# Kernel tuning notes

Measured on AMD Instinct MI355X. Metric: run time of the kernel, lower is better.

Reference implementation:

```python
import jax, jax.numpy as jnp
import numpy as np

B, S, D, H = 2, 2048, 2048, 16
HD = D // H  # head_dim = 128


def setup_inputs() -> dict:
    key = jax.random.key(0)
    k1, k2, k3, k4, k5, k6 = jax.random.split(key, 6)
    scale = 1.0 / np.sqrt(D)
    return {
        "hidden_states": jax.random.normal(k1, (B, S, D), dtype=jnp.float32),
        "attention_mask": jnp.ones((B, S), dtype=jnp.int32),
        "wq": jax.random.normal(k2, (D, D), dtype=jnp.float32) * scale,
        "wk": jax.random.normal(k3, (D, D), dtype=jnp.float32) * scale,
        "wv": jax.random.normal(k4, (D, D), dtype=jnp.float32) * scale,
        "wo": jax.random.normal(k5, (D, D), dtype=jnp.float32) * scale,
        "bo": jax.random.normal(k6, (D,), dtype=jnp.float32) * 0.01,
    }


def reference(hidden_states, attention_mask, wq, wk, wv, wo, bo):
    b, s, d = hidden_states.shape
    # QKV projections (no bias), split heads -> [B, S, H, HD]
    q = (hidden_states @ wq).reshape(b, s, H, HD)
    k = (hidden_states @ wk).reshape(b, s, H, HD)
    v = (hidden_states @ wv).reshape(b, s, H, HD)

    # combined causal + padding mask -> [B, 1, S, S]
    causal = jnp.tril(jnp.ones((s, s), dtype=bool))[None, None]
    pad = (attention_mask > 0)[:, None, None, :]  # [B,1,1,S]
    mask = jnp.logical_and(causal, pad)

    big_neg = jnp.finfo(hidden_states.dtype).min
    bias = jnp.where(mask, 0.0, big_neg).astype(hidden_states.dtype)

    # scaled dot-product attention (flax dot_product_attention scales by 1/sqrt(head_dim))
    scores = jnp.einsum("bqhd,bkhd->bhqk", q, k) / jnp.sqrt(jnp.asarray(HD, hidden_states.dtype))
    probs = jax.nn.softmax(scores + bias, axis=-1)
    ctx = jnp.einsum("bhqk,bkhd->bqhd", probs, v).reshape(b, s, d)

    return ctx @ wo + bo
```

## Files before the change

kernel.cpp:

```cpp
#include <hip/hip_runtime.h>
#include <hip/hip_bf16.h>
#include <stdint.h>

#define Bv 2
#define Sv 2048
#define Dv 2048
#define Hv 16
#define HDv 128
#define Mv (Bv*Sv)

typedef __attribute__((ext_vector_type(8))) short short8;
typedef __attribute__((ext_vector_type(4))) short short4v;
typedef __attribute__((ext_vector_type(4))) float f32x4;

__device__ __forceinline__ unsigned short bf16_rne(float f) {
    union { float f; uint32_t u; } c; c.f = f;
    uint32_t u = c.u;
    u += 0x7fffu + ((u >> 16) & 1u);
    return (unsigned short)(u >> 16);
}

__device__ __forceinline__ uint32_t cvt_pk_bf16(float lo, float hi) {
    uint32_t r;
    asm("v_cvt_pk_bf16_f32 %0, %1, %2" : "=v"(r) : "v"(lo), "v"(hi));
    return r;
}

__device__ __forceinline__ void gload16(const void* g, void* l) {
    __builtin_amdgcn_global_load_lds((const __attribute__((address_space(1))) void*)g,
                                     (__attribute__((address_space(3))) void*)l, 16, 0, 0);
}

#define BARRIER() asm volatile("s_barrier" ::: "memory")
#define LGKM0()   do { asm volatile("s_waitcnt lgkmcnt(0)" ::: "memory"); \
                       __builtin_amdgcn_sched_barrier(0); } while (0)

__global__ void cvt_x_kernel(const float* __restrict__ x, unsigned short* __restrict__ xb) {
    int i = (blockIdx.x * 256 + threadIdx.x) * 4;
    float4 v = *(const float4*)(x + i);
    short4v o;
    o[0] = (short)bf16_rne(v.x);
    o[1] = (short)bf16_rne(v.y);
    o[2] = (short)bf16_rne(v.z);
    o[3] = (short)bf16_rne(v.w);
    *(short4v*)(xb + i) = o;
}

__global__ void cvt_wt_kernel(const float* __restrict__ w0, const float* __restrict__ w1,
                              const float* __restrict__ w2, const float* __restrict__ w3,
                              unsigned short* __restrict__ wt) {
    __shared__ unsigned short t[64][65];
    int z = blockIdx.z;
    const float* w = (z == 0) ? w0 : (z == 1) ? w1 : (z == 2) ? w2 : w3;
    unsigned short* o = wt + (size_t)z * Dv * Dv;
    int k0 = blockIdx.x * 64, n0 = blockIdx.y * 64;
    for (int i = threadIdx.x; i < 4096; i += 256) {
        int r = i >> 6, c = i & 63;
        t[r][c] = bf16_rne(w[(size_t)(k0 + r) * Dv + n0 + c]);
    }
    __syncthreads();
    for (int i = threadIdx.x; i < 4096; i += 256) {
        int r = i >> 6, c = i & 63;
        o[(size_t)(n0 + r) * Dv + k0 + c] = t[c][r];
    }
}

__global__ void vt_kernel(const unsigned short* __restrict__ V, unsigned short* __restrict__ VT) {
    __shared__ unsigned short t[64 * 64];
    const int tid = threadIdx.x;
    const int b = blockIdx.z;
    const int s0 = blockIdx.x * 64, c0 = blockIdx.y * 64;
    const unsigned short* Vb = V + (size_t)b * Sv * Dv;
    unsigned short* VTb = VT + (size_t)b * Dv * Sv;
    #pragma unroll
    for (int ii = 0; ii < 2; ++ii) {
        int i = tid + ii * 256;
        int r = i >> 3, ch = i & 7;
        short8 v = *(const short8*)&Vb[(size_t)(s0 + r) * Dv + c0 + ch * 8];
        *(short8*)&t[r * 64 + ((ch ^ (r & 7)) << 3)] = v;
    }
    __syncthreads();
    #pragma unroll
    for (int ii = 0; ii < 2; ++ii) {
        int o = tid + ii * 256;
        int orow = o >> 3, och = o & 7;
        short8 v;
        #pragma unroll
        for (int j = 0; j < 8; ++j) {
            int r = och * 8 + j;
            int c = orow;
            v[j] = (short)t[r * 64 + ((((c >> 3) ^ (r & 7)) << 3) | (c & 7))];
        }
        *(short8*)&VTb[(size_t)(c0 + orow) * Sv + s0 + och * 8] = v;
    }
}

__global__ __launch_bounds__(512, 2) void gemm8ph_kernel(
    const unsigned short* __restrict__ A,
    const unsigned short* __restrict__ WtBase,
    unsigned short* __restrict__ CbBase)
{
    extern __shared__ unsigned short lds[];
    const int tid = threadIdx.x;
    const int wv = tid >> 6, ln = tid & 63;
    const int lr = ln & 15, lg = ln >> 4;
    const int wm = wv >> 2, wn = wv & 3;

    const int bid = blockIdx.x;
    const int xcd = bid & 7, idx = bid >> 3;
    const int n_idx = xcd * 3 + idx / 16;
    const int m_idx = idx % 16;
    const int m0 = m_idx * 256, n0g = n_idx * 256;

    const int lrow = wv * 8 + (ln >> 3);
    const int lcol = ((ln & 7) ^ (ln >> 3)) << 3;
    const unsigned short* Ag = A      + (size_t)(m0  + lrow) * Dv + lcol;
    const unsigned short* Bg = WtBase + (size_t)(n0g + lrow) * Dv + lcol;

    auto SH = [&](int T, int isB, int h) {
        const unsigned short* src = (isB ? Bg : Ag) + (size_t)(h * 128) * Dv + T * 64;
        unsigned short* dst = &lds[(T & 1) * 32768 + isB * 16384 + h * 8192 + wv * 512];
        gload16(src, dst);
        gload16(src + (size_t)64 * Dv, dst + 4096);
    };

    const int axk = lr & 7;
    auto RDA = [&](int buf, int fm, int ks) {
        return *(const short8*)&lds[buf * 32768 + (wm * 128 + fm * 16 + lr) * 64 + (((ks * 4 + lg) ^ axk) << 3)];
    };
    auto RDB = [&](int buf, int fn, int ks) {
        return *(const short8*)&lds[buf * 32768 + 16384 + (wn * 64 + fn * 16 + lr) * 64 + (((ks * 4 + lg) ^ axk) << 3)];
    };

    f32x4 acc[8][4];
    #pragma unroll
    for (int fm = 0; fm < 8; fm++)
        #pragma unroll
        for (int fn = 0; fn < 4; fn++)
            acc[fm][fn] = (f32x4){0.f, 0.f, 0.f, 0.f};

    SH(0, 0, 0); SH(0, 0, 1); SH(0, 1, 0); SH(0, 1, 1);
    SH(1, 1, 0); SH(1, 0, 0);
    asm volatile("s_waitcnt vmcnt(4)" ::: "memory");
    BARRIER();

    short8 af[8], b0[4], b1[4];
    const int NT2 = 16;

    #define MFMA_BLK(FN0, FN1, BARR) do {                                              \
        __builtin_amdgcn_s_setprio(1);                                                 \
        _Pragma("unroll")                                                              \
        for (int fm = 0; fm < 8; fm++) {                                               \
            acc[fm][FN0] = __builtin_amdgcn_mfma_f32_16x16x32_bf16(af[fm], BARR[FN0], acc[fm][FN0], 0, 0, 0); \
            acc[fm][FN1] = __builtin_amdgcn_mfma_f32_16x16x32_bf16(af[fm], BARR[FN1], acc[fm][FN1], 0, 0, 0); \
        }                                                                              \
        __builtin_amdgcn_s_setprio(0);                                                 \
    } while (0)

    for (int i = 0; i < NT2; ++i) {
        const int Tb = 2 * i + 1;
        const bool more = (i + 1 < NT2);

        #pragma unroll
        for (int fm = 0; fm < 8; fm++) af[fm] = RDA(0, fm, 0);
        #pragma unroll
        for (int fn = 0; fn < 4; fn++) b0[fn] = RDB(0, fn, 0);
        SH(Tb, 0, 1);
        BARRIER(); LGKM0();
        MFMA_BLK(0, 1, b0);
        BARRIER();

        #pragma unroll
        for (int fn = 0; fn < 4; fn++) b1[fn] = RDB(0, fn, 1);
        SH(Tb, 1, 1);
        BARRIER(); LGKM0();
        MFMA_BLK(2, 3, b0);
        BARRIER();

        #pragma unroll
        for (int fm = 0; fm < 8; fm++) af[fm] = RDA(0, fm, 1);
        if (more) SH(Tb + 1, 1, 0);
        BARRIER(); LGKM0();
        MFMA_BLK(0, 1, b1);
        BARRIER();

        if (more) SH(Tb + 1, 0, 0);
        BARRIER(); LGKM0();
        MFMA_BLK(2, 3, b1);
        if (more) asm volatile("s_waitcnt vmcnt(4)" ::: "memory");
        else      asm volatile("s_waitcnt vmcnt(0)" ::: "memory");
        BARRIER();

        #pragma unroll
        for (int fm = 0; fm < 8; fm++) af[fm] = RDA(1, fm, 0);
        #pragma unroll
        for (int fn = 0; fn < 4; fn++) b0[fn] = RDB(1, fn, 0);
        if (more) SH(Tb + 1, 0, 1);
        BARRIER(); LGKM0();
        MFMA_BLK(0, 1, b0);
        BARRIER();

        #pragma unroll
        for (int fn = 0; fn < 4; fn++) b1[fn] = RDB(1, fn, 1);
        if (more) SH(Tb + 1, 1, 1);
        BARRIER(); LGKM0();
        MFMA_BLK(2, 3, b0);
        BARRIER();

        #pragma unroll
        for (int fm = 0; fm < 8; fm++) af[fm] = RDA(1, fm, 1);
        if (more) SH(Tb + 2, 1, 0);
        BARRIER(); LGKM0();
        MFMA_BLK(0, 1, b1);
        BARRIER();

        if (more) SH(Tb + 2, 0, 0);
        BARRIER(); LGKM0();
        MFMA_BLK(2, 3, b1);
        if (more) {
            asm volatile("s_waitcnt vmcnt(4)" ::: "memory");
            BARRIER();
        }
    }
    #undef MFMA_BLK

    const int z = n0g >> 11;
    unsigned short* Cz = CbBase + (size_t)z * Mv * Dv;
    const int ncl = (n0g & 2047) + wn * 64;
    #pragma unroll
    for (int fm = 0; fm < 8; fm++)
        #pragma unroll
        for (int fn = 0; fn < 4; fn++) {
            int row = m0 + wm * 128 + fm * 16 + lg * 4;
            int col = ncl + fn * 16 + lr;
            #pragma unroll
            for (int r = 0; r < 4; r++)
                Cz[(size_t)(row + r) * Dv + col] = bf16_rne(acc[fm][fn][r]);
        }
}

__global__ __launch_bounds__(512, 2) void gemm8_kernel(
    const unsigned short* __restrict__ A,
    const unsigned short* __restrict__ WtBase,
    float* __restrict__ Cf,
    const float* __restrict__ bias)
{
    extern __shared__ unsigned short lds[];
    const int tid = threadIdx.x;
    const int wv = tid >> 6, ln = tid & 63;
    const int lr = ln & 15, lg = ln >> 4;
    const int wm = wv >> 2, wn = wv & 3;

    const int bid = blockIdx.x;
    const int xcd = bid & 7, idx = bid >> 3;
    const int n_idx = xcd;
    const int m_idx = idx;
    const int m0 = m_idx * 128;
    const int n0g = n_idx * 256;
    const int NT = Dv / 64;

    const int srow = ln >> 3;
    const int swz = ((ln & 7) ^ srow) << 3;
    const unsigned short* Ab = A      + (size_t)(m0  + wv * 8 + srow) * Dv + swz;
    const unsigned short* Bb = WtBase + (size_t)(n0g + wv * 8 + srow) * Dv + swz;

    auto STAGE_A = [&](int t, int d) {
        const unsigned short* g = Ab + t * 64;
        #pragma unroll
        for (int j = 0; j < 2; ++j)
            gload16(g + (size_t)(j * 64) * Dv, &lds[d * 24576 + (j * 64 + wv * 8) * 64]);
    };
    auto STAGE_B = [&](int t, int d) {
        const unsigned short* g = Bb + t * 64;
        #pragma unroll
        for (int j = 0; j < 4; ++j)
            gload16(g + (size_t)(j * 64) * Dv, &lds[d * 24576 + 8192 + (j * 64 + wv * 8) * 64]);
    };

    const int aro = (wm * 64 + lr) * 64;
    const int bro = (wn * 64 + lr) * 64;
    const int ach0 = ((lg ^ (lr & 7)) << 3);
    const int ach1 = (((4 + lg) ^ (lr & 7)) << 3);

    f32x4 acc[4][4];
    #pragma unroll
    for (int mi = 0; mi < 4; mi++)
        #pragma unroll
        for (int ni = 0; ni < 4; ni++)
            acc[mi][ni] = (f32x4){0.f, 0.f, 0.f, 0.f};

    STAGE_A(0, 0); STAGE_B(0, 0);
    STAGE_A(1, 1); STAGE_B(1, 1);
    asm volatile("s_waitcnt vmcnt(6)" ::: "memory");
    BARRIER();

    for (int t = 0; t < NT; ++t) {
        const int d = t % 3, d2 = (t + 2) % 3;
        const unsigned short* la = &lds[d * 24576];
        const unsigned short* lb = &lds[d * 24576 + 8192];

        short8 af[4][2], bf0[2][2];
        #pragma unroll
        for (int mi = 0; mi < 4; mi++) {
            af[mi][0] = *(const short8*)&la[aro + mi * 1024 + ach0];
            af[mi][1] = *(const short8*)&la[aro + mi * 1024 + ach1];
        }
        #pragma unroll
        for (int ni = 0; ni < 2; ni++) {
            bf0[ni][0] = *(const short8*)&lb[bro + ni * 1024 + ach0];
            bf0[ni][1] = *(const short8*)&lb[bro + ni * 1024 + ach1];
        }
        if (t + 2 < NT) STAGE_A(t + 2, d2);
        BARRIER();
        __builtin_amdgcn_s_setprio(1);
        #pragma unroll
        for (int mi = 0; mi < 4; mi++)
            #pragma unroll
            for (int ni = 0; ni < 2; ni++) {
                acc[mi][ni] = __builtin_amdgcn_mfma_f32_16x16x32_bf16(af[mi][0], bf0[ni][0], acc[mi][ni], 0, 0, 0);
                acc[mi][ni] = __builtin_amdgcn_mfma_f32_16x16x32_bf16(af[mi][1], bf0[ni][1], acc[mi][ni], 0, 0, 0);
            }
        __builtin_amdgcn_s_setprio(0);

        short8 bf1[2][2];
        #pragma unroll
        for (int ni = 0; ni < 2; ni++) {
            bf1[ni][0] = *(const short8*)&lb[bro + (ni + 2) * 1024 + ach0];
            bf1[ni][1] = *(const short8*)&lb[bro + (ni + 2) * 1024 + ach1];
        }
        if (t + 2 < NT) STAGE_B(t + 2, d2);
        asm volatile("s_waitcnt vmcnt(6)" ::: "memory");
        BARRIER();
        __builtin_amdgcn_s_setprio(1);
        #pragma unroll
        for (int mi = 0; mi < 4; mi++)
            #pragma unroll
            for (int ni = 0; ni < 2; ni++) {
                acc[mi][ni + 2] = __builtin_amdgcn_mfma_f32_16x16x32_bf16(af[mi][0], bf1[ni][0], acc[mi][ni + 2], 0, 0, 0);
                acc[mi][ni + 2] = __builtin_amdgcn_mfma_f32_16x16x32_bf16(af[mi][1], bf1[ni][1], acc[mi][ni + 2], 0, 0, 0);
            }
        __builtin_amdgcn_s_setprio(0);
    }

    #pragma unroll
    for (int mi = 0; mi < 4; mi++)
        #pragma unroll
        for (int ni = 0; ni < 4; ni++) {
            int row = m0 + wm * 64 + mi * 16 + lg * 4;
            int col = n0g + wn * 64 + ni * 16 + lr;
            float bv = bias[col];
            #pragma unroll
            for (int r = 0; r < 4; r++)
                Cf[(size_t)(row + r) * Dv + col] = acc[mi][ni][r] + bv;
        }
}

__global__ __launch_bounds__(512) void attn_kernel(
    const unsigned short* __restrict__ Q, const unsigned short* __restrict__ K,
    const unsigned short* __restrict__ VT, const int* __restrict__ pmask,
    unsigned short* __restrict__ CTX)
{
    __shared__ unsigned short lK[2][64 * 128];
    __shared__ unsigned short lVt[2][128 * 64];
    __shared__ int lPmB[2][64];
    __shared__ int lPmOk[2];

    const int tid = threadIdx.x, wv = tid >> 6, ln = tid & 63;
    const int lr = ln & 15, lg = ln >> 4;
    const int L = blockIdx.x;
    const int bh = (L & 7) * 4 + ((L >> 3) & 3);
    const int b = bh >> 4, h = bh & 15;
    const int v = L >> 5;
    const int qidx = (v < 8) ? (15 - v) : (v - 8);
    const int q0 = qidx * 128;
    const int qw0 = q0 + wv * 16;
    const size_t hoff  = (size_t)b * Sv * Dv + (size_t)h * HDv;
    const size_t vtoff = ((size_t)b * Dv + (size_t)h * HDv) * Sv;

    short8 qf[4];
    #pragma unroll
    for (int ds = 0; ds < 4; ds++)
        qf[ds] = *(const short8*)&Q[hoff + (size_t)(qw0 + lr) * Dv + ds * 32 + lg * 8];

    size_t koff[2], voff[2];
    #pragma unroll
    for (int ii = 0; ii < 2; ++ii) {
        int slot = ii * 512 + wv * 64 + ln;
        int krow = slot >> 4, kch = slot & 15;
        koff[ii] = hoff + (size_t)krow * Dv + ((kch ^ (krow & 7)) << 3);
        int vrow = slot >> 3, vch = slot & 7;
        voff[ii] = vtoff + (size_t)vrow * Sv + ((vch ^ (vrow & 7)) << 3);
    }

    auto STAGE = [&](int t, int buf) {
        const size_t kadd = (size_t)(t << 6) * Dv;
        const int vadd = t << 6;
        unsigned short* kb = &lK[buf][0];
        unsigned short* vb = &lVt[buf][0];
        #pragma unroll
        for (int ii = 0; ii < 2; ++ii) {
            gload16(K + koff[ii] + kadd, kb + (ii * 512 + wv * 64) * 8);
            gload16(VT + voff[ii] + vadd, vb + (ii * 512 + wv * 64) * 8);
        }
        if (wv == 0) {
            int pmv = pmask[b * Sv + (t << 6) + ln];
            lPmB[buf][ln] = pmv;
            unsigned long long bal = __ballot(pmv != 0);
            if (ln == 0) lPmOk[buf] = (bal == ~0ull) ? 1 : 0;
        }
    };

    f32x4 acc[8];
    #pragma unroll
    for (int n = 0; n < 8; n++) acc[n] = (f32x4){0.f, 0.f, 0.f, 0.f};
    float mrow = -3.0e38f, lrow = 0.f;
    const float CS = 0.12751744f;
    const int qg = qw0 + lr;
    const int nt = (q0 >> 6) + 2;
    const int srcA = lr + ((lg & 1) << 5);
    const int srcB = srcA + 16;
    const bool hiSel = (lg >= 2);

    auto TILE = [&](int t, int buf, auto CAUSAL_c) {
        constexpr bool CAUSAL = decltype(CAUSAL_c)::value;
        const int kv0 = t << 6;
        const unsigned short* kb = &lK[buf][0];
        const unsigned short* vb = &lVt[buf][0];

        f32x4 st[4];
        #pragma unroll
        for (int t2 = 0; t2 < 4; ++t2) st[t2] = (f32x4){0.f, 0.f, 0.f, 0.f};
        __builtin_amdgcn_s_setprio(1);
        #pragma unroll
        for (int t2 = 0; t2 < 4; ++t2) {
            const int krow = t2 * 16 + lr;
            #pragma unroll
            for (int ds = 0; ds < 4; ++ds) {
                const int ch = ds * 4 + lg;
                short8 kf = *(const short8*)&kb[krow * 128 + ((ch ^ (krow & 7)) << 3)];
                st[t2] = __builtin_amdgcn_mfma_f32_16x16x32_bf16(kf, qf[ds], st[t2], 0, 0, 0);
            }
        }
        __builtin_amdgcn_s_setprio(0);

        float sv[4][4];
        float rmax;
        if constexpr (CAUSAL) {
            const int* pm = &lPmB[buf][0];
            #pragma unroll
            for (int t2 = 0; t2 < 4; ++t2)
                #pragma unroll
                for (int r = 0; r < 4; ++r) {
                    int kvl = t2 * 16 + lg * 4 + r;
                    bool ok = ((kv0 + kvl) <= qg) && (pm[kvl] != 0);
                    sv[t2][r] = ok ? st[t2][r] * CS : -1.0e30f;
                }
            rmax = sv[0][0];
            #pragma unroll
            for (int t2 = 0; t2 < 4; ++t2)
                #pragma unroll
                for (int r = 0; r < 4; ++r) rmax = fmaxf(rmax, sv[t2][r]);
            rmax = fmaxf(rmax, __shfl_xor(rmax, 16, 64));
            rmax = fmaxf(rmax, __shfl_xor(rmax, 32, 64));
        } else {
            rmax = st[0][0];
            #pragma unroll
            for (int t2 = 0; t2 < 4; ++t2)
                #pragma unroll
                for (int r = 0; r < 4; ++r) rmax = fmaxf(rmax, st[t2][r]);
            rmax = fmaxf(rmax, __shfl_xor(rmax, 16, 64));
            rmax = fmaxf(rmax, __shfl_xor(rmax, 32, 64));
            rmax *= CS;
        }

        if (!__all(rmax - mrow <= 8.0f)) {
            float mn = fmaxf(mrow, rmax);
            float alpha = exp2f(mrow - mn);
            mrow = mn;
            lrow *= alpha;
            #pragma unroll
            for (int n = 0; n < 8; n++)
                #pragma unroll
                for (int r = 0; r < 4; r++) acc[n][r] *= alpha;
        }

        float p[4][4]; float psum = 0.f;
        if constexpr (CAUSAL) {
            #pragma unroll
            for (int t2 = 0; t2 < 4; ++t2)
                #pragma unroll
                for (int r = 0; r < 4; ++r) {
                    float e = exp2f(sv[t2][r] - mrow);
                    p[t2][r] = (sv[t2][r] > -5.0e29f) ? e : 0.f;
                    psum += p[t2][r];
                }
        } else {
            if (lPmOk[buf]) {
                #pragma unroll
                for (int t2 = 0; t2 < 4; ++t2)
                    #pragma unroll
                    for (int r = 0; r < 4; ++r) {
                        p[t2][r] = exp2f(fmaf(st[t2][r], CS, -mrow));
                        psum += p[t2][r];
                    }
            } else {
                const int* pm = &lPmB[buf][0];
                #pragma unroll
                for (int t2 = 0; t2 < 4; ++t2)
                    #pragma unroll
                    for (int r = 0; r < 4; ++r) {
                        int kvl = t2 * 16 + lg * 4 + r;
                        float e = exp2f(fmaf(st[t2][r], CS, -mrow));
                        p[t2][r] = (pm[kvl] != 0) ? e : 0.f;
                        psum += p[t2][r];
                    }
            }
        }
        psum += __shfl_xor(psum, 16, 64);
        psum += __shfl_xor(psum, 32, 64);
        lrow += psum;

        uint32_t pk[4][2];
        #pragma unroll
        for (int t2 = 0; t2 < 4; ++t2)
            #pragma unroll
            for (int pp = 0; pp < 2; ++pp)
                pk[t2][pp] = cvt_pk_bf16(p[t2][2 * pp], p[t2][2 * pp + 1]);

        union U { uint32_t u[4]; short8 s; } pa0, pa1;
        {
            uint32_t l0 = (uint32_t)__shfl((int)pk[0][0], srcA, 64), h0 = (uint32_t)__shfl((int)pk[1][0], srcA, 64);
            uint32_t l1 = (uint32_t)__shfl((int)pk[0][1], srcA, 64), h1 = (uint32_t)__shfl((int)pk[1][1], srcA, 64);
            uint32_t l2 = (uint32_t)__shfl((int)pk[0][0], srcB, 64), h2 = (uint32_t)__shfl((int)pk[1][0], srcB, 64);
            uint32_t l3 = (uint32_t)__shfl((int)pk[0][1], srcB, 64), h3 = (uint32_t)__shfl((int)pk[1][1], srcB, 64);
            pa0.u[0] = hiSel ? h0 : l0; pa0.u[1] = hiSel ? h1 : l1;
            pa0.u[2] = hiSel ? h2 : l2; pa0.u[3] = hiSel ? h3 : l3;
        }
        {
            uint32_t l0 = (uint32_t)__shfl((int)pk[2][0], srcA, 64), h0 = (uint32_t)__shfl((int)pk[3][0], srcA, 64);
            uint32_t l1 = (uint32_t)__shfl((int)pk[2][1], srcA, 64), h1 = (uint32_t)__shfl((int)pk[3][1], srcA, 64);
            uint32_t l2 = (uint32_t)__shfl((int)pk[2][0], srcB, 64), h2 = (uint32_t)__shfl((int)pk[3][0], srcB, 64);
            uint32_t l3 = (uint32_t)__shfl((int)pk[2][1], srcB, 64), h3 = (uint32_t)__shfl((int)pk[3][1], srcB, 64);
            pa1.u[0] = hiSel ? h0 : l0; pa1.u[1] = hiSel ? h1 : l1;
            pa1.u[2] = hiSel ? h2 : l2; pa1.u[3] = hiSel ? h3 : l3;
        }

        __builtin_amdgcn_s_setprio(1);
        #pragma unroll
        for (int n = 0; n < 8; n++) {
            const int vrow = n * 16 + lr;
            short8 a0 = *(const short8*)&vb[vrow * 64 + ((lg ^ (vrow & 7)) << 3)];
            acc[n] = __builtin_amdgcn_mfma_f32_16x16x32_bf16(a0, pa0.s, acc[n], 0, 0, 0);
            short8 a1 = *(const short8*)&vb[vrow * 64 + (((4 + lg) ^ (vrow & 7)) << 3)];
            acc[n] = __builtin_amdgcn_mfma_f32_16x16x32_bf16(a1, pa1.s, acc[n], 0, 0, 0);
        }
        __builtin_amdgcn_s_setprio(0);
    };

    STAGE(0, 0);
    __syncthreads();
    int cur = 0;

    for (int t = 0; t < nt; ++t) {
        if (t + 1 < nt) STAGE(t + 1, cur ^ 1);
        const int kv0 = t << 6;
        if (kv0 <= qw0 + 15) {
            if (kv0 + 63 > qw0) TILE(t, cur, std::integral_constant<bool, true>{});
            else                TILE(t, cur, std::integral_constant<bool, false>{});
        }
        __syncthreads();
        cur ^= 1;
    }

    float inv = 1.0f / lrow;
    #pragma unroll
    for (int n = 0; n < 8; n++) {
        short4v o;
        #pragma unroll
        for (int r = 0; r < 4; r++) o[r] = (short)bf16_rne(acc[n][r] * inv);
        *(short4v*)&CTX[hoff + (size_t)qg * Dv + n * 16 + lg * 4] = o;
    }
}

extern "C" void kernel_launch(void* const* d_in, const int* in_sizes, int n_in,
                              void* d_out, int out_size, void* d_ws, size_t ws_size,
                              hipStream_t stream) {
    const float* hs  = (const float*)d_in[0];
    const int*   am  = (const int*)d_in[1];
    const float* wq  = (const float*)d_in[2];
    const float* wk  = (const float*)d_in[3];
    const float* wv_ = (const float*)d_in[4];
    const float* wo  = (const float*)d_in[5];
    const float* bo  = (const float*)d_in[6];
    float* out = (float*)d_out;

    char* ws = (char*)d_ws;
    unsigned short* Xb  = (unsigned short*)ws;
    unsigned short* Wt  = (unsigned short*)(ws + (size_t)16 * 1024 * 1024);
    unsigned short* QKV = (unsigned short*)(ws + (size_t)48 * 1024 * 1024);
    unsigned short* CTX = (unsigned short*)(ws + (size_t)96 * 1024 * 1024);
    unsigned short* VT  = Xb;

    const int LDSB_8PH = 131072;
    const int LDSB_OUT = 147456;
    static bool attrSet = false;
    if (!attrSet) {
        hipFuncSetAttribute((const void*)gemm8ph_kernel, hipFuncAttributeMaxDynamicSharedMemorySize, LDSB_8PH);
        hipFuncSetAttribute((const void*)gemm8_kernel, hipFuncAttributeMaxDynamicSharedMemorySize, LDSB_OUT);
        attrSet = true;
    }

    hipLaunchKernelGGL(cvt_x_kernel, dim3(Mv * Dv / 4 / 256), dim3(256), 0, stream, hs, Xb);
    hipLaunchKernelGGL(cvt_wt_kernel, dim3(32, 32, 4), dim3(256), 0, stream, wq, wk, wv_, wo, Wt);
    hipLaunchKernelGGL(gemm8ph_kernel, dim3(384), dim3(512), LDSB_8PH, stream, Xb, Wt, QKV);
    hipLaunchKernelGGL(vt_kernel, dim3(32, 32, 2), dim3(256), 0, stream,
                       QKV + 2 * (size_t)Mv * Dv, VT);
    hipLaunchKernelGGL(attn_kernel, dim3(512), dim3(512), 0, stream,
                       QKV, QKV + (size_t)Mv * Dv, VT, am, CTX);
    hipLaunchKernelGGL(gemm8_kernel, dim3(256), dim3(512), LDSB_OUT, stream,
                       CTX, Wt + 3 * (size_t)Dv * Dv, out, bo);
}
```

Baseline: 249.9 us.

## Retile QKV GEMM to 256x192 tiles with single-tile pipelined LDS stages

The QKV projection GEMM changes from 256x256 tiles on 384 blocks to 256x192 tiles on 512 blocks, so the grid maps evenly onto the CUs (two blocks per CU). The prefetch schedule is rebuilt around per-64-row A/B chunk loads with a smaller LDS footprint per stage. B tiles are loaded two tiles ahead and A one tile ahead. Output columns may now cross the Q/K/V boundary inside a tile, so z is computed per column. The narrower N-tile lowers arithmetic intensity per LDS byte and changes the wait counts, which risks exposing memory latency.

```diff
diff --git a/kernel.cpp b/kernel.cpp
--- a/kernel.cpp
+++ b/kernel.cpp
@@ -95,12 +95,16 @@
     }
 }
 
-__global__ __launch_bounds__(512, 2) void gemm8ph_kernel(
+__global__ __launch_bounds__(512, 2) void gemm8p_kernel(
     const unsigned short* __restrict__ A,
     const unsigned short* __restrict__ WtBase,
     unsigned short* __restrict__ CbBase)
 {
     extern __shared__ unsigned short lds[];
+    constexpr int SLOT = 28672;
+    constexpr int BOFF = 16384;
+    constexpr int NT = Dv / 64;
+
     const int tid = threadIdx.x;
     const int wv = tid >> 6, ln = tid & 63;
     const int lr = ln & 15, lg = ln >> 4;
@@ -108,131 +112,109 @@
 
     const int bid = blockIdx.x;
     const int xcd = bid & 7, idx = bid >> 3;
-    const int n_idx = xcd * 3 + idx / 16;
-    const int m_idx = idx % 16;
-    const int m0 = m_idx * 256, n0g = n_idx * 256;
+    const int n_idx = xcd * 4 + (idx >> 4);
+    const int m_idx = idx & 15;
+    const int m0 = m_idx * 256, n0g = n_idx * 192;
 
     const int lrow = wv * 8 + (ln >> 3);
     const int lcol = ((ln & 7) ^ (ln >> 3)) << 3;
     const unsigned short* Ag = A      + (size_t)(m0  + lrow) * Dv + lcol;
     const unsigned short* Bg = WtBase + (size_t)(n0g + lrow) * Dv + lcol;
 
-    auto SH = [&](int T, int isB, int h) {
-        const unsigned short* src = (isB ? Bg : Ag) + (size_t)(h * 128) * Dv + T * 64;
-        unsigned short* dst = &lds[(T & 1) * 32768 + isB * 16384 + h * 8192 + wv * 512];
-        gload16(src, dst);
-        gload16(src + (size_t)64 * Dv, dst + 4096);
+    auto SA = [&](int T, int j) {
+        gload16(Ag + (size_t)(j * 64) * Dv + T * 64, &lds[(T & 1) * SLOT + j * 4096 + wv * 512]);
+    };
+    auto SB = [&](int T, int j) {
+        gload16(Bg + (size_t)(j * 64) * Dv + T * 64, &lds[(T & 1) * SLOT + BOFF + j * 4096 + wv * 512]);
     };
 
     const int axk = lr & 7;
     auto RDA = [&](int buf, int fm, int ks) {
-        return *(const short8*)&lds[buf * 32768 + (wm * 128 + fm * 16 + lr) * 64 + (((ks * 4 + lg) ^ axk) << 3)];
+        return *(const short8*)&lds[buf * SLOT + (wm * 128 + fm * 16 + lr) * 64 + (((ks * 4 + lg) ^ axk) << 3)];
     };
     auto RDB = [&](int buf, int fn, int ks) {
-        return *(const short8*)&lds[buf * 32768 + 16384 + (wn * 64 + fn * 16 + lr) * 64 + (((ks * 4 + lg) ^ axk) << 3)];
-    };
-
-    f32x4 acc[8][4];
+        return *(const short8*)&lds[buf * SLOT + BOFF + (wn * 48 + fn * 16 + lr) * 64 + (((ks * 4 + lg) ^ axk) << 3)];
+    };
+
+    f32x4 acc[8][3];
     #pragma unroll
     for (int fm = 0; fm < 8; fm++)
         #pragma unroll
-        for (int fn = 0; fn < 4; fn++)
+        for (int fn = 0; fn < 3; fn++)
             acc[fm][fn] = (f32x4){0.f, 0.f, 0.f, 0.f};
 
-    SH(0, 0, 0); SH(0, 0, 1); SH(0, 1, 0); SH(0, 1, 1);
-    SH(1, 1, 0); SH(1, 0, 0);
-    asm volatile("s_waitcnt vmcnt(4)" ::: "memory");
+    SA(0, 0); SA(0, 1); SA(0, 2); SA(0, 3);
+    SB(0, 0); SB(0, 1); SB(0, 2);
+    SB(1, 0); SB(1, 1); SB(1, 2);
+    asm volatile("s_waitcnt vmcnt(3)" ::: "memory");
     BARRIER();
 
-    short8 af[8], b0[4], b1[4];
-    const int NT2 = 16;
-
-    #define MFMA_BLK(FN0, FN1, BARR) do {                                              \
-        __builtin_amdgcn_s_setprio(1);                                                 \
-        _Pragma("unroll")                                                              \
-        for (int fm = 0; fm < 8; fm++) {                                               \
-            acc[fm][FN0] = __builtin_amdgcn_mfma_f32_16x16x32_bf16(af[fm], BARR[FN0], acc[fm][FN0], 0, 0, 0); \
-            acc[fm][FN1] = __builtin_amdgcn_mfma_f32_16x16x32_bf16(af[fm], BARR[FN1], acc[fm][FN1], 0, 0, 0); \
-        }                                                                              \
-        __builtin_amdgcn_s_setprio(0);                                                 \
+    #define MFMA12(AF, FB, BR) do {                                                     \
+        __builtin_amdgcn_s_setprio(1);                                                  \
+        _Pragma("unroll")                                                               \
+        for (int fm = 0; fm < 4; fm++)                                                  \
+            _Pragma("unroll")                                                           \
+            for (int fn = 0; fn < 3; fn++)                                              \
+                acc[FB + fm][fn] = __builtin_amdgcn_mfma_f32_16x16x32_bf16(AF[fm], BR[fn], acc[FB + fm][fn], 0, 0, 0); \
+        __builtin_amdgcn_s_setprio(0);                                                  \
     } while (0)
 
-    for (int i = 0; i < NT2; ++i) {
-        const int Tb = 2 * i + 1;
-        const bool more = (i + 1 < NT2);
-
-        #pragma unroll
-        for (int fm = 0; fm < 8; fm++) af[fm] = RDA(0, fm, 0);
-        #pragma unroll
-        for (int fn = 0; fn < 4; fn++) b0[fn] = RDB(0, fn, 0);
-        SH(Tb, 0, 1);
+    auto TILEBODY = [&](int t, int buf) {
+        short8 af[4], b0[3], b1[3];
+        const bool s1 = (t + 1 < NT), s2 = (t + 2 < NT);
+
+        #pragma unroll
+        for (int f = 0; f < 4; f++) af[f] = RDA(buf, f, 0);
+        #pragma unroll
+        for (int f = 0; f < 3; f++) b0[f] = RDB(buf, f, 0);
+        if (s1) { SA(t + 1, 0); SA(t + 1, 1); }
         BARRIER(); LGKM0();
-        MFMA_BLK(0, 1, b0);
+        MFMA12(af, 0, b0);
         BARRIER();
 
-        #pragma unroll
-        for (int fn = 0; fn < 4; fn++) b1[fn] = RDB(0, fn, 1);
-        SH(Tb, 1, 1);
+        short8 ah[4];
+        #pragma unroll
+        for (int f = 0; f < 4; f++) ah[f] = RDA(buf, 4 + f, 0);
+        if (s1) SA(t + 1, 2);
         BARRIER(); LGKM0();
-        MFMA_BLK(2, 3, b0);
+        MFMA12(ah, 4, b0);
         BARRIER();
 
         #pragma unroll
-        for (int fm = 0; fm < 8; fm++) af[fm] = RDA(0, fm, 1);
-        if (more) SH(Tb + 1, 1, 0);
+        for (int f = 0; f < 4; f++) af[f] = RDA(buf, f, 1);
+        #pragma unroll
+        for (int f = 0; f < 3; f++) b1[f] = RDB(buf, f, 1);
+        if (s1) SA(t + 1, 3);
         BARRIER(); LGKM0();
-        MFMA_BLK(0, 1, b1);
+        MFMA12(af, 0, b1);
         BARRIER();
 
-        if (more) SH(Tb + 1, 0, 0);
+        #pragma unroll
+        for (int f = 0; f < 4; f++) ah[f] = RDA(buf, 4 + f, 1);
+        if (s2) { SB(t + 2, 0); SB(t + 2, 1); SB(t + 2, 2); }
         BARRIER(); LGKM0();
-        MFMA_BLK(2, 3, b1);
-        if (more) asm volatile("s_waitcnt vmcnt(4)" ::: "memory");
-        else      asm volatile("s_waitcnt vmcnt(0)" ::: "memory");
+        MFMA12(ah, 4, b1);
+        if (s2)      asm volatile("s_waitcnt vmcnt(3)" ::: "memory");
+        else if (s1) asm volatile("s_waitcnt vmcnt(0)" ::: "memory");
         BARRIER();
-
-        #pragma unroll
-        for (int fm = 0; fm < 8; fm++) af[fm] = RDA(1, fm, 0);
-        #pragma unroll
-        for (int fn = 0; fn < 4; fn++) b0[fn] = RDB(1, fn, 0);
-        if (more) SH(Tb + 1, 0, 1);
-        BARRIER(); LGKM0();
-        MFMA_BLK(0, 1, b0);
-        BARRIER();
-
-        #pragma unroll
-        for (int fn = 0; fn < 4; fn++) b1[fn] = RDB(1, fn, 1);
-        if (more) SH(Tb + 1, 1, 1);
-        BARRIER(); LGKM0();
-        MFMA_BLK(2, 3, b0);
-        BARRIER();
-
-        #pragma unroll
-        for (int fm = 0; fm < 8; fm++) af[fm] = RDA(1, fm, 1);
-        if (more) SH(Tb + 2, 1, 0);
-        BARRIER(); LGKM0();
-        MFMA_BLK(0, 1, b1);
-        BARRIER();
-
-        if (more) SH(Tb + 2, 0, 0);
-        BARRIER(); LGKM0();
-        MFMA_BLK(2, 3, b1);
-        if (more) {
-            asm volatile("s_waitcnt vmcnt(4)" ::: "memory");
-            BARRIER();
-        }
-    }
-    #undef MFMA_BLK
-
-    const int z = n0g >> 11;
-    unsigned short* Cz = CbBase + (size_t)z * Mv * Dv;
-    const int ncl = (n0g & 2047) + wn * 64;
+    };
+
+    #pragma unroll 1
+    for (int i = 0; i < NT / 2; ++i) {
+        TILEBODY(2 * i, 0);
+        TILEBODY(2 * i + 1, 1);
+    }
+    #undef MFMA12
+
     #pragma unroll
     for (int fm = 0; fm < 8; fm++)
         #pragma unroll
-        for (int fn = 0; fn < 4; fn++) {
-            int row = m0 + wm * 128 + fm * 16 + lg * 4;
-            int col = ncl + fn * 16 + lr;
+        for (int fn = 0; fn < 3; fn++) {
+            int row  = m0 + wm * 128 + fm * 16 + lg * 4;
+            int colg = n0g + wn * 48 + fn * 16 + lr;
+            int z    = colg >> 11;
+            int col  = colg & 2047;
+            unsigned short* Cz = CbBase + (size_t)z * Mv * Dv;
             #pragma unroll
             for (int r = 0; r < 4; r++)
                 Cz[(size_t)(row + r) * Dv + col] = bf16_rne(acc[fm][fn][r]);
@@ -601,18 +583,18 @@
     unsigned short* CTX = (unsigned short*)(ws + (size_t)96 * 1024 * 1024);
     unsigned short* VT  = Xb;
 
-    const int LDSB_8PH = 131072;
+    const int LDSB_8P  = 114688;
     const int LDSB_OUT = 147456;
     static bool attrSet = false;
     if (!attrSet) {
-        hipFuncSetAttribute((const void*)gemm8ph_kernel, hipFuncAttributeMaxDynamicSharedMemorySize, LDSB_8PH);
+        hipFuncSetAttribute((const void*)gemm8p_kernel, hipFuncAttributeMaxDynamicSharedMemorySize, LDSB_8P);
         hipFuncSetAttribute((const void*)gemm8_kernel, hipFuncAttributeMaxDynamicSharedMemorySize, LDSB_OUT);
         attrSet = true;
     }
 
     hipLaunchKernelGGL(cvt_x_kernel, dim3(Mv * Dv / 4 / 256), dim3(256), 0, stream, hs, Xb);
     hipLaunchKernelGGL(cvt_wt_kernel, dim3(32, 32, 4), dim3(256), 0, stream, wq, wk, wv_, wo, Wt);
-    hipLaunchKernelGGL(gemm8ph_kernel, dim3(384), dim3(512), LDSB_8PH, stream, Xb, Wt, QKV);
+    hipLaunchKernelGGL(gemm8p_kernel, dim3(512), dim3(512), LDSB_8P, stream, Xb, Wt, QKV);
     hipLaunchKernelGGL(vt_kernel, dim3(32, 32, 2), dim3(256), 0, stream,
                        QKV + 2 * (size_t)Mv * Dv, VT);
     hipLaunchKernelGGL(attn_kernel, dim3(512), dim3(512), 0, stream,
```

Measured after the change: 238.5 us. 4.6% less time.
